# Kernel optimization log

Hardware: AMD Instinct MI355X
Metric: run time of the kernel (lower is better)

The kernel has to match this reference:

```python
import jax, jax.numpy as jnp
import numpy as np

WINDOWS = (5, 10, 20)
EPS = 1e-8


def _rolling_sum(x, w):
    # S[t] = sum(x[max(0, t-w+1) : t+1]) via prefix sums
    T = x.shape[1]
    cs = jnp.cumsum(x, axis=1)
    shifted = jnp.pad(cs, ((0, 0), (w, 0)))[:, :T]  # cs[t-w] (0 for t<w)
    return cs - shifted


def _window_count(T, w, dtype):
    return jnp.minimum(jnp.arange(T) + 1, w).astype(dtype)  # [T]


def _rolling_mean(x, w):
    cnt = _window_count(x.shape[1], w, x.dtype)
    return _rolling_sum(x, w) / cnt


def _rolling_std(x, w):
    # unbiased (ddof=1) std over the trailing window; 1e-6 when count < 2
    T = x.shape[1]
    cnt = _window_count(T, w, x.dtype)
    s = _rolling_sum(x, w)
    sq = _rolling_sum(x * x, w)
    var = (sq - s * s / cnt) / jnp.maximum(cnt - 1.0, 1.0)
    std = jnp.sqrt(jnp.maximum(var, 0.0))
    std = jnp.where(jnp.isnan(std), 1e-6, std)
    return jnp.where(cnt >= 2.0, std, 1e-6)


def _shift(x, n):
    # result[:, n:] = x[:, :-n]; result[:, :n] = x[:, 0:1]
    return jnp.concatenate([jnp.repeat(x[:, :1], n, axis=1), x[:, :-n]], axis=1)


def _rolling_bipower(r, w):
    # bv[t] = (pi/2) * sum_{i=t-w}^{t-2} |r_i||r_{i+1}|, zero for t < w
    B, T = r.shape
    p = jnp.abs(r[:, :-1]) * jnp.abs(r[:, 1:])                  # [B, T-1]
    P = jnp.pad(jnp.cumsum(p, axis=1), ((0, 0), (1, 0)))        # P[k] = sum p[:k], [B, T]
    a = jnp.pad(P, ((0, 0), (1, 0)))[:, :T]                     # P[t-1]
    b = jnp.pad(P, ((0, 0), (w, 0)))[:, :T]                     # P[t-w]
    bv = (a - b) * (np.pi / 2.0)
    mask = (jnp.arange(T) >= w).astype(r.dtype)
    return bv * mask


def regime_features(prices):
    log_prices = jnp.log(prices + EPS)
    returns = jnp.pad(log_prices[:, 1:] - log_prices[:, :-1], ((0, 0), (1, 0)))

    feats = [_rolling_std(returns, w) for w in WINDOWS]

    sma_s = _rolling_mean(prices, 5)
    sma_l = _rolling_mean(prices, 20)
    feats.append((sma_s - sma_l) / (sma_l + EPS))

    shifted = _shift(prices, 5)
    feats.append((prices - shifted) / (shifted + EPS))

    bv = _rolling_bipower(returns, 20)
    rv = _rolling_std(returns, 20) ** 2
    feats.append(rv / (bv + EPS))

    return jnp.stack(feats, axis=-1)  # [B, T, 6]


def setup_inputs() -> dict:
    key = jax.random.key(0)
    B, T = 1024, 8192
    z = jax.random.normal(key, (B, T), dtype=jnp.float32)
    # GBM-like positive price paths around 100
    prices = 100.0 * jnp.exp(0.01 * jnp.cumsum(z, axis=1))
    return {"prices": prices}


def reference(prices):
    return regime_features(prices)
```

## Files before the change

kernel.cpp:

```cpp
#include <hip/hip_runtime.h>
#include <math.h>


constexpr int BLOCK = 256;
constexpr int RPT   = 4;
constexpr int CHUNK = BLOCK * RPT;
constexpr int HALO  = 21;
constexpr int NS    = CHUNK + HALO;
#define PIDX2(e) ((e) + ((e) >> 5))
constexpr int LDSF  = CHUNK * 6;
constexpr float EPS = 1e-8f;
constexpr float PI_HALF = 1.5707963267948966f;
constexpr float LN2 = 0.6931471805599453f;

typedef float f32x4 __attribute__((ext_vector_type(4)));

__device__ __forceinline__ float frcp(float x) { return __builtin_amdgcn_rcpf(x); }
__device__ __forceinline__ float fsq(float x)  { return __builtin_amdgcn_sqrtf(x); }

__global__ __launch_bounds__(BLOCK, 6)
void regime_kernel(const float* __restrict__ prices, float* __restrict__ out, int T) {
    __shared__ __align__(16) float lds[LDSF];
    float2* const srp = (float2*)lds;

    const int tid = threadIdx.x;
    const int t0  = blockIdx.x * CHUNK;
    const int row = blockIdx.y;
    const float* __restrict__ pr = prices + (size_t)row * T;

    for (int i = tid; i < NS; i += BLOCK) {
        int g = t0 - HALO + i;
        float p = (g >= 0) ? pr[g] : 0.0f;
        float r = 0.0f;
        if (g >= 1) {
            float pm = pr[g - 1];
            r = (__builtin_amdgcn_logf(p + EPS) - __builtin_amdgcn_logf(pm + EPS)) * LN2;
        }
        srp[PIDX2(i)] = make_float2(r, p);
    }
    __syncthreads();

    const int tf = t0 + tid * RPT;
    const int lf = HALO + tid * RPT;

    float s5 = 0.f, q5 = 0.f, ps5 = 0.f;
    float s10 = 0.f, q10 = 0.f;
    float s20 = 0.f, q20 = 0.f, ps20 = 0.f;
    float A = 0.f, aprev = 0.f;
    float aA = 0.f, aB = 0.f, aprev20 = 0.f;
    float p0 = 0.f, p5v = 0.f;
    float  r10s[3];
    float2 s5s[3];
    float2 s20s[3];

    #pragma unroll
    for (int i = 20; i >= 0; --i) {
        float2 v = srp[PIDX2(lf - i)];
        float r = v.x, p = v.y;
        float a = fabsf(r);
        if (i == 20) { aprev20 = a; aprev = a; }
        else if (i >= 1) { A = fmaf(aprev, a, A); aprev = a; }
        if (i == 1) aA = a;
        if (i == 0) aB = a;
        if (i >= 7  && i <= 9)  r10s[9 - i]  = r;
        if (i >= 2  && i <= 4)  s5s[4 - i]   = v;
        if (i >= 17 && i <= 19) s20s[19 - i] = v;
        if (i <= 19) {
            s20 += r; q20 = fmaf(r, r, q20);
            ps20 += p;
            if (i == 5) p5v = p;
            if (i == 0) p0 = p;
            if (i <= 9) { s10 += r; q10 = fmaf(r, r, q10); }
            if (i <= 4) { s5 += r; q5 = fmaf(r, r, q5); ps5 += p; }
        }
    }

    float fb[RPT * 6];
    float pt = p0, shifted = p5v;

    #pragma unroll
    for (int k = 0; k < RPT; ++k) {
        const int t = tf + k;
        if (k > 0) {
            float2 vn  = srp[PIDX2(lf + k)];
            float rn   = vn.x;
            float r5o  = s5s[k - 1].x;
            float r10o = r10s[k - 1];
            float2 v20 = s20s[k - 1];
            float rn2 = rn * rn;
            s5  += rn - r5o;    q5  += rn2 - r5o  * r5o;
            s10 += rn - r10o;   q10 += rn2 - r10o * r10o;
            s20 += rn - v20.x;  q20 += rn2 - v20.x * v20.x;
            pt      = vn.y;
            shifted = s5s[k - 1].y;
            ps5  += pt - shifted;
            ps20 += pt - v20.y;
            A = fmaf(aA, aB, A);
            float a20n = fabsf(v20.x);
            A = fmaf(-aprev20, a20n, A);
            aprev20 = a20n;
            aA = aB; aB = fabsf(rn);
        }

        float c5r, c10r, c20r, d5r, d10r, d20r;
        if (t >= 19) {
            c5r = 0.2f; c10r = 0.1f; c20r = 0.05f;
            d5r = 0.25f; d10r = 1.f / 9.f; d20r = 1.f / 19.f;
        } else {
            int tp1 = t + 1;
            float c5  = (float)(tp1 < 5  ? tp1 : 5);
            float c10 = (float)(tp1 < 10 ? tp1 : 10);
            float c20 = (float)tp1;
            c5r  = frcp(c5);  c10r = frcp(c10);  c20r = frcp(c20);
            d5r  = frcp(fmaxf(c5  - 1.f, 1.f));
            d10r = frcp(fmaxf(c10 - 1.f, 1.f));
            d20r = frcp(fmaxf(c20 - 1.f, 1.f));
        }

        float var5  = (q5  - s5  * s5  * c5r ) * d5r;
        float var10 = (q10 - s10 * s10 * c10r) * d10r;
        float var20 = (q20 - s20 * s20 * c20r) * d20r;
        float std5  = fsq(fmaxf(var5,  0.f));
        float std10 = fsq(fmaxf(var10, 0.f));
        float std20 = fsq(fmaxf(var20, 0.f));
        const bool has2 = (t >= 1);
        float f1 = has2 ? std5  : 1e-6f;
        float f2 = has2 ? std10 : 1e-6f;
        float f3 = has2 ? std20 : 1e-6f;

        float m5  = ps5  * c5r;
        float m20 = ps20 * c20r;
        float f4 = (m5 - m20) * frcp(m20 + EPS);

        float sh = (t >= 5) ? shifted : srp[PIDX2(HALO)].y;
        float f5 = (pt - sh) * frcp(sh + EPS);

        float rvv = f3 * f3;
        float bv = (t >= 20) ? A * PI_HALF : 0.f;
        float f6 = rvv * frcp(bv + EPS);

        fb[k * 6 + 0] = f1; fb[k * 6 + 1] = f2; fb[k * 6 + 2] = f3;
        fb[k * 6 + 3] = f4; fb[k * 6 + 4] = f5; fb[k * 6 + 5] = f6;
    }

    __syncthreads();
    f32x4* const ost4 = (f32x4*)lds;
    #pragma unroll
    for (int m = 0; m < 6; ++m) {
        int g = 6 * tid + m;
        int p = g ^ ((g >> 3) & 7);
        f32x4 v = { fb[4 * m], fb[4 * m + 1], fb[4 * m + 2], fb[4 * m + 3] };
        ost4[p] = v;
    }
    __syncthreads();

    f32x4* __restrict__ outp4 = (f32x4*)(out + ((size_t)row * T + t0) * 6);
    #pragma unroll
    for (int r = 0; r < 6; ++r) {
        int g = r * BLOCK + tid;
        int p = g ^ ((g >> 3) & 7);
        outp4[g] = ost4[p];
    }
}

extern "C" void kernel_launch(void* const* d_in, const int* in_sizes, int n_in,
                              void* d_out, int out_size, void* d_ws, size_t ws_size,
                              hipStream_t stream) {
    const float* prices = (const float*)d_in[0];
    float* out = (float*)d_out;
    const int T = 8192;
    const int B = in_sizes[0] / T;
    dim3 grid(T / CHUNK, B);
    hipLaunchKernelGGL(regime_kernel, grid, dim3(BLOCK), 0, stream, prices, out, T);
}
```

Baseline: 51.93 us.

## Load price window directly into registers, dropping LDS staging and sync

Each thread now loads its own 28-element price window with vector loads straight into registers and computes log returns locally, replacing the cooperative LDS staging pass and one barrier. The LN2 scaling is folded into the final std and bipower constants instead of being applied per return. Launch bounds occupancy hint drops from 6 to 4 to allow more registers. The cost is redundant global loads (each thread re-reads a 24-element halo, about 7x the data via cache) and about 24 logs per thread instead of roughly one.

Measured after the change: 42.26 us, median of 2. 18.6% less time.

```diff
diff --git a/kernel.cpp b/kernel.cpp
--- a/kernel.cpp
+++ b/kernel.cpp
@@ -5,43 +5,45 @@
 constexpr int BLOCK = 256;
 constexpr int RPT   = 4;
 constexpr int CHUNK = BLOCK * RPT;
-constexpr int HALO  = 21;
-constexpr int NS    = CHUNK + HALO;
-#define PIDX2(e) ((e) + ((e) >> 5))
 constexpr int LDSF  = CHUNK * 6;
 constexpr float EPS = 1e-8f;
-constexpr float PI_HALF = 1.5707963267948966f;
 constexpr float LN2 = 0.6931471805599453f;
+constexpr float PI_HALF_L2SQ = 1.5707963267948966f * LN2 * LN2;
 
 typedef float f32x4 __attribute__((ext_vector_type(4)));
 
-__device__ __forceinline__ float frcp(float x) { return __builtin_amdgcn_rcpf(x); }
-__device__ __forceinline__ float fsq(float x)  { return __builtin_amdgcn_sqrtf(x); }
+__device__ __forceinline__ float frcp(float x)  { return __builtin_amdgcn_rcpf(x); }
+__device__ __forceinline__ float fsq(float x)   { return __builtin_amdgcn_sqrtf(x); }
+__device__ __forceinline__ float flog2(float x) { return __builtin_amdgcn_logf(x); }
 
-__global__ __launch_bounds__(BLOCK, 6)
+__global__ __launch_bounds__(BLOCK, 4)
 void regime_kernel(const float* __restrict__ prices, float* __restrict__ out, int T) {
     __shared__ __align__(16) float lds[LDSF];
-    float2* const srp = (float2*)lds;
+    f32x4* const ost4 = (f32x4*)lds;
 
     const int tid = threadIdx.x;
     const int t0  = blockIdx.x * CHUNK;
     const int row = blockIdx.y;
     const float* __restrict__ pr = prices + (size_t)row * T;
 
-    for (int i = tid; i < NS; i += BLOCK) {
-        int g = t0 - HALO + i;
-        float p = (g >= 0) ? pr[g] : 0.0f;
-        float r = 0.0f;
-        if (g >= 1) {
-            float pm = pr[g - 1];
-            r = (__builtin_amdgcn_logf(p + EPS) - __builtin_amdgcn_logf(pm + EPS)) * LN2;
-        }
-        srp[PIDX2(i)] = make_float2(r, p);
+    const int tf = t0 + tid * RPT;
+    const float p0row = pr[0];
+
+    f32x4 L[7];
+    if (tf >= 24) {
+        const f32x4* __restrict__ src = (const f32x4*)(pr + (tf - 24));
+        #pragma unroll
+        for (int m = 0; m < 7; ++m) L[m] = src[m];
+    } else {
+        #pragma unroll
+        for (int m = 0; m < 7; ++m)
+            #pragma unroll
+            for (int e = 0; e < 4; ++e) {
+                int g = tf - 24 + 4 * m + e;
+                float v = pr[g > 0 ? g : 0];
+                L[m][e] = (g >= 0) ? v : 0.0f;
+            }
     }
-    __syncthreads();
-
-    const int tf = t0 + tid * RPT;
-    const int lf = HALO + tid * RPT;
 
     float s5 = 0.f, q5 = 0.f, ps5 = 0.f;
     float s10 = 0.f, q10 = 0.f;
@@ -49,25 +51,29 @@
     float A = 0.f, aprev = 0.f;
     float aA = 0.f, aB = 0.f, aprev20 = 0.f;
     float p0 = 0.f, p5v = 0.f;
-    float  r10s[3];
-    float2 s5s[3];
-    float2 s20s[3];
+    float r10s[3], vnr[3], vnp[3];
+    float2 s5s[3], s20s[3];
 
+    float lp_prev = flog2(L[0][3] + EPS);
     #pragma unroll
-    for (int i = 20; i >= 0; --i) {
-        float2 v = srp[PIDX2(lf - i)];
-        float r = v.x, p = v.y;
+    for (int j = 4; j < 28; ++j) {
+        float p  = L[j >> 2][j & 3];
+        float lp = flog2(p + EPS);
+        float r  = lp - lp_prev;
+        lp_prev = lp;
+        if (tf < 24 && (tf - 24 + j) < 1) r = 0.0f;
         float a = fabsf(r);
+        const int i = 24 - j;
         if (i == 20) { aprev20 = a; aprev = a; }
         else if (i >= 1) { A = fmaf(aprev, a, A); aprev = a; }
         if (i == 1) aA = a;
         if (i == 0) aB = a;
         if (i >= 7  && i <= 9)  r10s[9 - i]  = r;
-        if (i >= 2  && i <= 4)  s5s[4 - i]   = v;
-        if (i >= 17 && i <= 19) s20s[19 - i] = v;
-        if (i <= 19) {
-            s20 += r; q20 = fmaf(r, r, q20);
-            ps20 += p;
+        if (i >= 2  && i <= 4)  s5s[4 - i]   = make_float2(r, p);
+        if (i >= 17 && i <= 19) s20s[19 - i] = make_float2(r, p);
+        if (i <= -1) { vnr[-i - 1] = r; vnp[-i - 1] = p; }
+        if (i >= 0 && i <= 19) {
+            s20 += r; q20 = fmaf(r, r, q20); ps20 += p;
             if (i == 5) p5v = p;
             if (i == 0) p0 = p;
             if (i <= 9) { s10 += r; q10 = fmaf(r, r, q10); }
@@ -82,8 +88,7 @@
     for (int k = 0; k < RPT; ++k) {
         const int t = tf + k;
         if (k > 0) {
-            float2 vn  = srp[PIDX2(lf + k)];
-            float rn   = vn.x;
+            float rn   = vnr[k - 1];
             float r5o  = s5s[k - 1].x;
             float r10o = r10s[k - 1];
             float2 v20 = s20s[k - 1];
@@ -91,7 +96,7 @@
             s5  += rn - r5o;    q5  += rn2 - r5o  * r5o;
             s10 += rn - r10o;   q10 += rn2 - r10o * r10o;
             s20 += rn - v20.x;  q20 += rn2 - v20.x * v20.x;
-            pt      = vn.y;
+            pt      = vnp[k - 1];
             shifted = s5s[k - 1].y;
             ps5  += pt - shifted;
             ps20 += pt - v20.y;
@@ -120,9 +125,9 @@
         float var5  = (q5  - s5  * s5  * c5r ) * d5r;
         float var10 = (q10 - s10 * s10 * c10r) * d10r;
         float var20 = (q20 - s20 * s20 * c20r) * d20r;
-        float std5  = fsq(fmaxf(var5,  0.f));
-        float std10 = fsq(fmaxf(var10, 0.f));
-        float std20 = fsq(fmaxf(var20, 0.f));
+        float std5  = fsq(fmaxf(var5,  0.f)) * LN2;
+        float std10 = fsq(fmaxf(var10, 0.f)) * LN2;
+        float std20 = fsq(fmaxf(var20, 0.f)) * LN2;
         const bool has2 = (t >= 1);
         float f1 = has2 ? std5  : 1e-6f;
         float f2 = has2 ? std10 : 1e-6f;
@@ -132,19 +137,17 @@
         float m20 = ps20 * c20r;
         float f4 = (m5 - m20) * frcp(m20 + EPS);
 
-        float sh = (t >= 5) ? shifted : srp[PIDX2(HALO)].y;
+        float sh = (t >= 5) ? shifted : p0row;
         float f5 = (pt - sh) * frcp(sh + EPS);
 
         float rvv = f3 * f3;
-        float bv = (t >= 20) ? A * PI_HALF : 0.f;
+        float bv = (t >= 20) ? A * PI_HALF_L2SQ : 0.f;
         float f6 = rvv * frcp(bv + EPS);
 
         fb[k * 6 + 0] = f1; fb[k * 6 + 1] = f2; fb[k * 6 + 2] = f3;
         fb[k * 6 + 3] = f4; fb[k * 6 + 4] = f5; fb[k * 6 + 5] = f6;
     }
 
-    __syncthreads();
-    f32x4* const ost4 = (f32x4*)lds;
     #pragma unroll
     for (int m = 0; m < 6; ++m) {
         int g = 6 * tid + m;
```
